# Performance work log

Hardware: AMD Instinct MI355X
Metric: run time of the kernel (lower is better)

Reference implementation:

```python
import jax, jax.numpy as jnp
import numpy as np

N_NODES = 100000
N_EDGES = 1600000
IN_DIM, HID_DIM, OUT_DIM = 32, 64, 8


def sage_conv(x, src, dst, W_l, b_l, W_r, n_nodes):
    # PyG SAGEConv (aggr='mean', root_weight=True):
    # out_i = W_l @ mean_{j in N(i)} x_j + b_l + W_r @ x_i
    msg_sum = jax.ops.segment_sum(x[src], dst, num_segments=n_nodes)  # [N, F]
    deg = jax.ops.segment_sum(jnp.ones((src.shape[0],), x.dtype), dst,
                              num_segments=n_nodes)  # [N]
    agg = msg_sum / jnp.maximum(deg, 1.0)[:, None]
    return agg @ W_l.T + b_l + x @ W_r.T


def setup_inputs() -> dict:
    key = jax.random.key(0)
    ks = jax.random.split(key, 8)
    x = jax.random.normal(ks[0], (N_NODES, IN_DIM), dtype=jnp.float32)
    edge_index = jax.random.randint(ks[1], (2, N_EDGES), 0, N_NODES, dtype=jnp.int64)
    s1 = 1.0 / np.sqrt(IN_DIM)
    s2 = 1.0 / np.sqrt(HID_DIM)
    return {
        "x": x,
        "edge_index": edge_index,
        "W1_l": jax.random.uniform(ks[2], (HID_DIM, IN_DIM), jnp.float32, -s1, s1),
        "b1": jnp.zeros((HID_DIM,), jnp.float32),
        "W1_r": jax.random.uniform(ks[3], (HID_DIM, IN_DIM), jnp.float32, -s1, s1),
        "W2_l": jax.random.uniform(ks[4], (OUT_DIM, HID_DIM), jnp.float32, -s2, s2),
        "b2": jnp.zeros((OUT_DIM,), jnp.float32),
        "W2_r": jax.random.uniform(ks[5], (OUT_DIM, HID_DIM), jnp.float32, -s2, s2),
    }


def reference(x, edge_index, W1_l, b1, W1_r, W2_l, b2, W2_r):
    src, dst = edge_index[0], edge_index[1]
    h = sage_conv(x, src, dst, W1_l, b1, W1_r, N_NODES)
    h = jax.nn.relu(h)
    out = sage_conv(h, src, dst, W2_l, b2, W2_r, N_NODES)
    return out
```

## Files before the change

kernel.cpp:

```cpp
#include <hip/hip_runtime.h>

#define N_NODES 100000
#define N_EDGES 1600000
#define IN_DIM 32
#define HID_DIM 64
#define OUT_DIM 8
#define CAP 64
#define CHUNK 4096
#define NCHUNK ((N_EDGES + CHUNK - 1) / CHUNK)
#define SLICE_W (N_NODES / 8)
#define QCAP 262144
#define BBLK 2048

typedef unsigned short u16;
typedef unsigned int u32;
typedef unsigned long long ull;

__device__ __forceinline__ float bf2f(u16 v) {
    return __uint_as_float(((u32)v) << 16);
}

__device__ __forceinline__ u16 f2bf(float f) {
    u32 u = __float_as_uint(f);
    u32 lsb = (u >> 16) & 1u;
    u += 0x7fffu + lsb;
    return (u16)(u >> 16);
}

__device__ __forceinline__ float ldf(const void* p, size_t i, int bf) {
    return bf ? bf2f(((const u16*)p)[i]) : ((const float*)p)[i];
}

__global__ __launch_bounds__(256) void k_part(
    const int* __restrict__ ei, const u32* __restrict__ xw,
    const void* __restrict__ W1l, const void* __restrict__ b1,
    const void* __restrict__ W1r,
    const void* __restrict__ W2l, const void* __restrict__ b2,
    const void* __restrict__ W2r,
    int* __restrict__ qcnt, u32* __restrict__ qbuf,
    int* __restrict__ cnt,
    float* __restrict__ tW1l, float* __restrict__ tW1r,
    float* __restrict__ tW2l, float* __restrict__ tW2r,
    float* __restrict__ tb1, float* __restrict__ tb2)
{
    __shared__ int shv, bfv;
    __shared__ int hist[4][8], wbase[4][8], lcur[4][8], gbase[8];
    int t = threadIdx.x, w = t >> 6;
    if (t < 64) {
        int v = ei[2 * t + 1];
        ull m1 = __ballot(v == 0);
        u32 wd = xw[t];
        u32 b = (wd >> 8) & 0x7fu;
        ull m2 = __ballot(b >= 0x38u && b <= 0x41u);
        if (t == 0) {
            shv = (m1 == ~0ULL) ? 1 : 0;
            bfv = (__popcll(m2) >= 56) ? 1 : 0;
        }
    }
    if (t < 32) { hist[t >> 3][t & 7] = 0; lcur[t >> 3][t & 7] = 0; }
    __syncthreads();
    int sh = shv, bf = bfv;

    for (int i = blockIdx.x * 256 + t; i < N_NODES; i += NCHUNK * 256) cnt[i] = 0;

    if (blockIdx.x < 16) {
        for (int i = blockIdx.x * 256 + t; i < HID_DIM * IN_DIM; i += 16 * 256) {
            int o = i / IN_DIM, k = i % IN_DIM;
            tW1l[k * HID_DIM + o] = ldf(W1l, i, bf);
            tW1r[k * HID_DIM + o] = ldf(W1r, i, bf);
        }
        for (int i = blockIdx.x * 256 + t; i < OUT_DIM * HID_DIM; i += 16 * 256) {
            int o = i / HID_DIM, k = i % HID_DIM;
            tW2l[k * OUT_DIM + o] = ldf(W2l, i, bf);
            tW2r[k * OUT_DIM + o] = ldf(W2r, i, bf);
        }
        if (blockIdx.x == 0) {
            if (t < HID_DIM) tb1[t] = ldf(b1, t, bf);
            if (t < OUT_DIM) tb2[t] = ldf(b2, t, bf);
        }
    }

    int e0 = blockIdx.x * CHUNK;
    int myd[16], mys[16];
    #pragma unroll
    for (int i = 0; i < 16; i++) {
        int e = e0 + i * 256 + t;
        if (e < N_EDGES) {
            size_t off = (size_t)e << sh;
            mys[i] = ei[off];
            int d = ei[((size_t)N_EDGES << sh) + off];
            myd[i] = d;
            atomicAdd(&hist[w][d / SLICE_W], 1);
        } else myd[i] = -1;
    }
    __syncthreads();
    if (t < 8) {
        int tot = hist[0][t] + hist[1][t] + hist[2][t] + hist[3][t];
        gbase[t] = atomicAdd(&qcnt[t], tot);
    }
    __syncthreads();
    if (t < 32) {
        int w2 = t >> 3, s = t & 7;
        int p = gbase[s];
        for (int w3 = 0; w3 < w2; w3++) p += hist[w3][s];
        wbase[w2][s] = p;
    }
    __syncthreads();
    #pragma unroll
    for (int i = 0; i < 16; i++) {
        int d = myd[i];
        if (d >= 0) {
            int s = d / SLICE_W;
            int p = wbase[w][s] + atomicAdd(&lcur[w][s], 1);
            qbuf[(size_t)s * QCAP + p] = ((u32)mys[i] << 14) | (u32)(d - s * SLICE_W);
        }
    }
}

__global__ __launch_bounds__(256) void k_build2(
    const int* __restrict__ qcnt, const u32* __restrict__ qbuf,
    int* __restrict__ cnt, int* __restrict__ slot)
{
    int slice = blockIdx.x & 7, bi = blockIdx.x >> 3;
    int m = qcnt[slice];
    int lo = slice * SLICE_W;
    const u32* q = qbuf + (size_t)slice * QCAP;
    for (int i = bi * 256 + threadIdx.x; i < m; i += (BBLK / 8) * 256) {
        u32 u = q[i];
        int d = lo + (int)(u & 0x3FFFu);
        int s = (int)(u >> 14);
        int pos = atomicAdd(&cnt[d], 1);
        if (pos < CAP) slot[(size_t)d * CAP + pos] = s;
    }
}

__global__ __launch_bounds__(256, 8) void k_sage1(
    const void* __restrict__ x, const int* __restrict__ cnt,
    const int* __restrict__ slot,
    const float* __restrict__ tW1l, const float* __restrict__ tW1r,
    const float* __restrict__ tW2l, const float* __restrict__ tW2r,
    const float* __restrict__ tb1, const float* __restrict__ tb2,
    const int* __restrict__ flags_unused,
    u16* __restrict__ gbuf, float* __restrict__ rbuf,
    const u32* __restrict__ xw)
{
    __shared__ float aggbuf[8][IN_DIM];
    __shared__ float xbuf[8][IN_DIM];
    __shared__ float hbuf[8][HID_DIM + 1];
    __shared__ int bfv;

    int t = threadIdx.x;
    if (t < 64) {
        u32 wd = xw[t];
        u32 b = (wd >> 8) & 0x7fu;
        ull m2 = __ballot(b >= 0x38u && b <= 0x41u);
        if (t == 0) bfv = (__popcll(m2) >= 56) ? 1 : 0;
    }
    __syncthreads();
    int bf = bfv;
    int wid = t >> 6, lane = t & 63;
    int half = lane >> 5;
    int g2 = (lane >> 3) & 3;
    int l = lane & 7;
    int ns = wid * 2 + half;
    int n = blockIdx.x * 8 + ns;
    int deg = cnt[n];
    int cl = (deg < CAP) ? deg : CAP;
    const int* srow = slot + (size_t)n * CAP;

    float a0 = 0, a1 = 0, a2 = 0, a3 = 0;
    float c0 = 0, c1 = 0, c2 = 0, c3 = 0;
    float d0 = 0, d1 = 0, d2 = 0, d3 = 0;
    float e0 = 0, e1 = 0, e2 = 0, e3 = 0;
    int j = g2;
    for (; j + 12 < cl; j += 16) {
        int sA = srow[j];
        int sB = srow[j + 4];
        int sC = srow[j + 8];
        int sD = srow[j + 12];
        if (bf) {
            ushort4 vA = reinterpret_cast<const ushort4*>((const u16*)x + (size_t)sA * IN_DIM)[l];
            ushort4 vB = reinterpret_cast<const ushort4*>((const u16*)x + (size_t)sB * IN_DIM)[l];
            ushort4 vC = reinterpret_cast<const ushort4*>((const u16*)x + (size_t)sC * IN_DIM)[l];
            ushort4 vD = reinterpret_cast<const ushort4*>((const u16*)x + (size_t)sD * IN_DIM)[l];
            a0 += bf2f(vA.x); a1 += bf2f(vA.y); a2 += bf2f(vA.z); a3 += bf2f(vA.w);
            c0 += bf2f(vB.x); c1 += bf2f(vB.y); c2 += bf2f(vB.z); c3 += bf2f(vB.w);
            d0 += bf2f(vC.x); d1 += bf2f(vC.y); d2 += bf2f(vC.z); d3 += bf2f(vC.w);
            e0 += bf2f(vD.x); e1 += bf2f(vD.y); e2 += bf2f(vD.z); e3 += bf2f(vD.w);
        } else {
            float4 vA = reinterpret_cast<const float4*>((const float*)x + (size_t)sA * IN_DIM)[l];
            float4 vB = reinterpret_cast<const float4*>((const float*)x + (size_t)sB * IN_DIM)[l];
            float4 vC = reinterpret_cast<const float4*>((const float*)x + (size_t)sC * IN_DIM)[l];
            float4 vD = reinterpret_cast<const float4*>((const float*)x + (size_t)sD * IN_DIM)[l];
            a0 += vA.x; a1 += vA.y; a2 += vA.z; a3 += vA.w;
            c0 += vB.x; c1 += vB.y; c2 += vB.z; c3 += vB.w;
            d0 += vC.x; d1 += vC.y; d2 += vC.z; d3 += vC.w;
            e0 += vD.x; e1 += vD.y; e2 += vD.z; e3 += vD.w;
        }
    }
    for (; j + 4 < cl; j += 8) {
        int sA = srow[j];
        int sB = srow[j + 4];
        if (bf) {
            ushort4 vA = reinterpret_cast<const ushort4*>((const u16*)x + (size_t)sA * IN_DIM)[l];
            ushort4 vB = reinterpret_cast<const ushort4*>((const u16*)x + (size_t)sB * IN_DIM)[l];
            a0 += bf2f(vA.x); a1 += bf2f(vA.y); a2 += bf2f(vA.z); a3 += bf2f(vA.w);
            c0 += bf2f(vB.x); c1 += bf2f(vB.y); c2 += bf2f(vB.z); c3 += bf2f(vB.w);
        } else {
            float4 vA = reinterpret_cast<const float4*>((const float*)x + (size_t)sA * IN_DIM)[l];
            float4 vB = reinterpret_cast<const float4*>((const float*)x + (size_t)sB * IN_DIM)[l];
            a0 += vA.x; a1 += vA.y; a2 += vA.z; a3 += vA.w;
            c0 += vB.x; c1 += vB.y; c2 += vB.z; c3 += vB.w;
        }
    }
    if (j < cl) {
        int s = srow[j];
        if (bf) {
            ushort4 v = reinterpret_cast<const ushort4*>((const u16*)x + (size_t)s * IN_DIM)[l];
            a0 += bf2f(v.x); a1 += bf2f(v.y); a2 += bf2f(v.z); a3 += bf2f(v.w);
        } else {
            float4 v = reinterpret_cast<const float4*>((const float*)x + (size_t)s * IN_DIM)[l];
            a0 += v.x; a1 += v.y; a2 += v.z; a3 += v.w;
        }
    }
    a0 += c0 + d0 + e0;
    a1 += c1 + d1 + e1;
    a2 += c2 + d2 + e2;
    a3 += c3 + d3 + e3;
    a0 += __shfl_xor(a0, 8, 64);  a0 += __shfl_xor(a0, 16, 64);
    a1 += __shfl_xor(a1, 8, 64);  a1 += __shfl_xor(a1, 16, 64);
    a2 += __shfl_xor(a2, 8, 64);  a2 += __shfl_xor(a2, 16, 64);
    a3 += __shfl_xor(a3, 8, 64);  a3 += __shfl_xor(a3, 16, 64);
    if (g2 == 0) {
        aggbuf[ns][4 * l + 0] = a0; aggbuf[ns][4 * l + 1] = a1;
        aggbuf[ns][4 * l + 2] = a2; aggbuf[ns][4 * l + 3] = a3;
    } else if (g2 == 1) {
        float f0, f1, f2, f3;
        if (bf) {
            ushort4 v = reinterpret_cast<const ushort4*>((const u16*)x + (size_t)n * IN_DIM)[l];
            f0 = bf2f(v.x); f1 = bf2f(v.y); f2 = bf2f(v.z); f3 = bf2f(v.w);
        } else {
            float4 v = reinterpret_cast<const float4*>((const float*)x + (size_t)n * IN_DIM)[l];
            f0 = v.x; f1 = v.y; f2 = v.z; f3 = v.w;
        }
        xbuf[ns][4 * l + 0] = f0; xbuf[ns][4 * l + 1] = f1;
        xbuf[ns][4 * l + 2] = f2; xbuf[ns][4 * l + 3] = f3;
    }
    __syncthreads();

    float rd0 = 1.0f / fmaxf((float)__shfl(deg, 0, 64), 1.0f);
    float rd1 = 1.0f / fmaxf((float)__shfl(deg, 32, 64), 1.0f);
    int s0 = wid * 2, s1 = wid * 2 + 1;
    int o = lane;
    float bb = tb1[o];
    float acc0 = bb, acc1 = bb;
    #pragma unroll 8
    for (int k = 0; k < IN_DIM; k++) {
        float wl = tW1l[k * HID_DIM + o];
        float wr = tW1r[k * HID_DIM + o];
        acc0 += (aggbuf[s0][k] * rd0) * wl + xbuf[s0][k] * wr;
        acc1 += (aggbuf[s1][k] * rd1) * wl + xbuf[s1][k] * wr;
    }
    hbuf[s0][o] = fmaxf(acc0, 0.0f);
    hbuf[s1][o] = fmaxf(acc1, 0.0f);
    __syncthreads();

    float ga = 0.0f, ra = 0.0f;
    #pragma unroll 4
    for (int m = 0; m < 16; m++) {
        int k = g2 * 16 + m;
        float hv = hbuf[ns][k];
        ga += hv * tW2l[k * OUT_DIM + l];
        ra += hv * tW2r[k * OUT_DIM + l];
    }
    ga += __shfl_xor(ga, 8, 64);  ga += __shfl_xor(ga, 16, 64);
    ra += __shfl_xor(ra, 8, 64);  ra += __shfl_xor(ra, 16, 64);
    if (g2 == 0) {
        gbuf[(size_t)n * OUT_DIM + l] = f2bf(ga);
        rbuf[(size_t)n * OUT_DIM + l] = ra + tb2[l];
    }
}

__global__ __launch_bounds__(256) void k_sage3(
    const u16* __restrict__ gbuf, const float* __restrict__ rbuf,
    const int* __restrict__ cnt, const int* __restrict__ slot,
    const u32* __restrict__ xw, void* __restrict__ out)
{
    __shared__ int bfv;
    int t = threadIdx.x;
    if (t < 64) {
        u32 w = xw[t];
        u32 b = (w >> 8) & 0x7fu;
        ull m2 = __ballot(b >= 0x38u && b <= 0x41u);
        if (t == 0) bfv = (__popcll(m2) >= 56) ? 1 : 0;
    }
    __syncthreads();
    int grp = t >> 3, l = t & 7;
    int n = blockIdx.x * 32 + grp;
    int deg = cnt[n];
    int cl = (deg < CAP) ? deg : CAP;
    const int* srow = slot + (size_t)n * CAP;
    float a0 = 0.0f, a1 = 0.0f, a2 = 0.0f, a3 = 0.0f;
    int j = 0;
    for (; j + 3 < cl; j += 4) {
        int v0 = srow[j];
        int v1 = srow[j + 1];
        int v2 = srow[j + 2];
        int v3 = srow[j + 3];
        a0 += bf2f(gbuf[(size_t)v0 * OUT_DIM + l]);
        a1 += bf2f(gbuf[(size_t)v1 * OUT_DIM + l]);
        a2 += bf2f(gbuf[(size_t)v2 * OUT_DIM + l]);
        a3 += bf2f(gbuf[(size_t)v3 * OUT_DIM + l]);
    }
    for (; j < cl; j++) a0 += bf2f(gbuf[(size_t)srow[j] * OUT_DIM + l]);
    float res = (a0 + a1 + a2 + a3) / fmaxf((float)deg, 1.0f)
              + rbuf[(size_t)n * OUT_DIM + l];
    size_t oi = (size_t)n * OUT_DIM + l;
    if (bfv) ((u16*)out)[oi] = f2bf(res);
    else     ((float*)out)[oi] = res;
}

extern "C" void kernel_launch(void* const* d_in, const int* in_sizes, int n_in,
                              void* d_out, int out_size, void* d_ws, size_t ws_size,
                              hipStream_t stream) {
    const void* x   = d_in[0];
    const int*  ei  = (const int*)d_in[1];
    const void* W1l = d_in[2];
    const void* b1  = d_in[3];
    const void* W1r = d_in[4];
    const void* W2l = d_in[5];
    const void* b2  = d_in[6];
    const void* W2r = d_in[7];

    int* qcnt    = (int*)d_ws;
    int* cnt     = qcnt + 8;
    float* tW1l  = (float*)(cnt + N_NODES);
    float* tW1r  = tW1l + IN_DIM * HID_DIM;
    float* tW2l  = tW1r + IN_DIM * HID_DIM;
    float* tW2r  = tW2l + HID_DIM * OUT_DIM;
    float* tb1   = tW2r + HID_DIM * OUT_DIM;
    float* tb2   = tb1 + HID_DIM;
    int* slot    = (int*)(tb2 + OUT_DIM);
    u32* qbuf    = (u32*)(slot + (size_t)N_NODES * CAP);
    u16* gbuf    = (u16*)(qbuf + (size_t)8 * QCAP);
    float* rbuf  = (float*)(gbuf + (size_t)N_NODES * OUT_DIM);

    hipMemsetAsync(d_ws, 0, 8 * sizeof(int), stream);

    k_part<<<NCHUNK, 256, 0, stream>>>(ei, (const u32*)x,
                                       W1l, b1, W1r, W2l, b2, W2r,
                                       qcnt, qbuf, cnt,
                                       tW1l, tW1r, tW2l, tW2r, tb1, tb2);
    k_build2<<<BBLK, 256, 0, stream>>>(qcnt, qbuf, cnt, slot);
    k_sage1<<<N_NODES / 8, 256, 0, stream>>>(x, cnt, slot, tW1l, tW1r,
                                             tW2l, tW2r, tb1, tb2, nullptr,
                                             gbuf, rbuf, (const u32*)x);
    k_sage3<<<N_NODES / 32, 256, 0, stream>>>(gbuf, rbuf, cnt, slot,
                                              (const u32*)x, d_out);
}
```

Measured before the change: 253.5 us.

## Fuse all stages into one cooperative persistent kernel with grid syncs

Replaces the four-kernel pipeline (partition, slot build, layer-1 SAGE, layer-2 aggregation) with a single cooperative kernel of 1024 persistent blocks separated by grid.sync barriers. Edge partitioning now writes into per-block, per-slice segments sized by a fixed cap instead of using global queue counters, and counter zeroing moves into the kernel. The aim is to remove kernel launch gaps and the memset. The costs are that each stage is limited to the cooperative grid's occupancy and every grid barrier is a full stall. Edges beyond the per-segment cap of 384 would be silently dropped, and the old kernels remain as a fallback if the cooperative launch fails.

Result: slower. 860.3 us (+239.4%).

```diff
diff --git a/kernel.cpp b/kernel.cpp
--- a/kernel.cpp
+++ b/kernel.cpp
@@ -1,4 +1,7 @@
 #include <hip/hip_runtime.h>
+#include <hip/hip_cooperative_groups.h>
+
+namespace cg = cooperative_groups;
 
 #define N_NODES 100000
 #define N_EDGES 1600000
@@ -6,9 +9,11 @@
 #define HID_DIM 64
 #define OUT_DIM 8
 #define CAP 64
+#define NBLK 1024
+#define SLICE_W (N_NODES / 8)
+#define SEGCAP 384
 #define CHUNK 4096
 #define NCHUNK ((N_EDGES + CHUNK - 1) / CHUNK)
-#define SLICE_W (N_NODES / 8)
 #define QCAP 262144
 #define BBLK 2048
 
@@ -31,7 +36,263 @@
     return bf ? bf2f(((const u16*)p)[i]) : ((const float*)p)[i];
 }
 
-__global__ __launch_bounds__(256) void k_part(
+__global__ __launch_bounds__(256, 4) void k_all(
+    const int* __restrict__ ei, const u32* __restrict__ xw,
+    const void* __restrict__ x,
+    const void* __restrict__ W1l, const void* __restrict__ b1,
+    const void* __restrict__ W1r,
+    const void* __restrict__ W2l, const void* __restrict__ b2,
+    const void* __restrict__ W2r,
+    int* __restrict__ cnt, int* __restrict__ qcntPB, u32* __restrict__ qbuf,
+    int* __restrict__ slot,
+    float* __restrict__ tW1l, float* __restrict__ tW1r,
+    float* __restrict__ tW2l, float* __restrict__ tW2r,
+    float* __restrict__ tb1, float* __restrict__ tb2,
+    u16* __restrict__ gbuf, float* __restrict__ rbuf,
+    void* __restrict__ out)
+{
+    __shared__ int shv, bfv;
+    __shared__ int lcnt[8];
+    __shared__ float aggbuf[8][IN_DIM];
+    __shared__ float xbuf[8][IN_DIM];
+    __shared__ float hbuf[8][HID_DIM + 1];
+
+    cg::grid_group grid = cg::this_grid();
+    int t = threadIdx.x;
+    int bid = blockIdx.x;
+
+    if (t < 64) {
+        int v = ei[2 * t + 1];
+        ull m1 = __ballot(v == 0);
+        u32 wd = xw[t];
+        u32 b = (wd >> 8) & 0x7fu;
+        ull m2 = __ballot(b >= 0x38u && b <= 0x41u);
+        if (t == 0) {
+            shv = (m1 == ~0ULL) ? 1 : 0;
+            bfv = (__popcll(m2) >= 56) ? 1 : 0;
+        }
+    }
+    if (t < 8) lcnt[t] = 0;
+    __syncthreads();
+    int sh = shv, bf = bfv;
+
+    for (int i = bid * 256 + t; i < N_NODES; i += NBLK * 256) cnt[i] = 0;
+
+    if (bid < 16) {
+        for (int i = bid * 256 + t; i < HID_DIM * IN_DIM; i += 16 * 256) {
+            int o = i / IN_DIM, k = i % IN_DIM;
+            tW1l[k * HID_DIM + o] = ldf(W1l, i, bf);
+            tW1r[k * HID_DIM + o] = ldf(W1r, i, bf);
+        }
+        for (int i = bid * 256 + t; i < OUT_DIM * HID_DIM; i += 16 * 256) {
+            int o = i / HID_DIM, k = i % HID_DIM;
+            tW2l[k * OUT_DIM + o] = ldf(W2l, i, bf);
+            tW2r[k * OUT_DIM + o] = ldf(W2r, i, bf);
+        }
+        if (bid == 0) {
+            if (t < HID_DIM) tb1[t] = ldf(b1, t, bf);
+            if (t < OUT_DIM) tb2[t] = ldf(b2, t, bf);
+        }
+    }
+
+    {
+        int e_begin = (int)((long long)bid * N_EDGES / NBLK);
+        int e_end   = (int)((long long)(bid + 1) * N_EDGES / NBLK);
+        for (int e = e_begin + t; e < e_end; e += 256) {
+            size_t off = (size_t)e << sh;
+            int s = ei[off];
+            int d = ei[((size_t)N_EDGES << sh) + off];
+            int sl = d / SLICE_W;
+            int pos = atomicAdd(&lcnt[sl], 1);
+            if (pos < SEGCAP)
+                qbuf[((size_t)sl * NBLK + bid) * SEGCAP + pos] =
+                    ((u32)s << 14) | (u32)(d - sl * SLICE_W);
+        }
+        __syncthreads();
+        if (t < 8) {
+            int c = lcnt[t];
+            qcntPB[bid * 8 + t] = (c < SEGCAP) ? c : SEGCAP;
+        }
+    }
+    __threadfence();
+    grid.sync();
+
+    {
+        int slice = bid & 7;
+        int lo = slice * SLICE_W;
+        for (int sb = bid >> 3; sb < NBLK; sb += (NBLK / 8)) {
+            int m = qcntPB[sb * 8 + slice];
+            const u32* q = qbuf + ((size_t)slice * NBLK + sb) * SEGCAP;
+            for (int i = t; i < m; i += 256) {
+                u32 u = q[i];
+                int d = lo + (int)(u & 0x3FFFu);
+                int s = (int)(u >> 14);
+                int pos = atomicAdd(&cnt[d], 1);
+                if (pos < CAP) slot[(size_t)d * CAP + pos] = s;
+            }
+        }
+    }
+    __threadfence();
+    grid.sync();
+
+    {
+        int wid = t >> 6, lane = t & 63;
+        int half = lane >> 5;
+        int g2 = (lane >> 3) & 3;
+        int l = lane & 7;
+        int ns = wid * 2 + half;
+        for (int g = bid; g < N_NODES / 8; g += NBLK) {
+            int n = g * 8 + ns;
+            int deg = cnt[n];
+            int cl = (deg < CAP) ? deg : CAP;
+            const int* srow = slot + (size_t)n * CAP;
+
+            float a0 = 0, a1 = 0, a2 = 0, a3 = 0;
+            float c0 = 0, c1 = 0, c2 = 0, c3 = 0;
+            float d0 = 0, d1 = 0, d2 = 0, d3 = 0;
+            float e0 = 0, e1 = 0, e2 = 0, e3 = 0;
+            int j = g2;
+            for (; j + 12 < cl; j += 16) {
+                int sA = srow[j];
+                int sB = srow[j + 4];
+                int sC = srow[j + 8];
+                int sD = srow[j + 12];
+                if (bf) {
+                    ushort4 vA = reinterpret_cast<const ushort4*>((const u16*)x + (size_t)sA * IN_DIM)[l];
+                    ushort4 vB = reinterpret_cast<const ushort4*>((const u16*)x + (size_t)sB * IN_DIM)[l];
+                    ushort4 vC = reinterpret_cast<const ushort4*>((const u16*)x + (size_t)sC * IN_DIM)[l];
+                    ushort4 vD = reinterpret_cast<const ushort4*>((const u16*)x + (size_t)sD * IN_DIM)[l];
+                    a0 += bf2f(vA.x); a1 += bf2f(vA.y); a2 += bf2f(vA.z); a3 += bf2f(vA.w);
+                    c0 += bf2f(vB.x); c1 += bf2f(vB.y); c2 += bf2f(vB.z); c3 += bf2f(vB.w);
+                    d0 += bf2f(vC.x); d1 += bf2f(vC.y); d2 += bf2f(vC.z); d3 += bf2f(vC.w);
+                    e0 += bf2f(vD.x); e1 += bf2f(vD.y); e2 += bf2f(vD.z); e3 += bf2f(vD.w);
+                } else {
+                    float4 vA = reinterpret_cast<const float4*>((const float*)x + (size_t)sA * IN_DIM)[l];
+                    float4 vB = reinterpret_cast<const float4*>((const float*)x + (size_t)sB * IN_DIM)[l];
+                    float4 vC = reinterpret_cast<const float4*>((const float*)x + (size_t)sC * IN_DIM)[l];
+                    float4 vD = reinterpret_cast<const float4*>((const float*)x + (size_t)sD * IN_DIM)[l];
+                    a0 += vA.x; a1 += vA.y; a2 += vA.z; a3 += vA.w;
+                    c0 += vB.x; c1 += vB.y; c2 += vB.z; c3 += vB.w;
+                    d0 += vC.x; d1 += vC.y; d2 += vC.z; d3 += vC.w;
+                    e0 += vD.x; e1 += vD.y; e2 += vD.z; e3 += vD.w;
+                }
+            }
+            for (; j + 4 < cl; j += 8) {
+                int sA = srow[j];
+                int sB = srow[j + 4];
+                if (bf) {
+                    ushort4 vA = reinterpret_cast<const ushort4*>((const u16*)x + (size_t)sA * IN_DIM)[l];
+                    ushort4 vB = reinterpret_cast<const ushort4*>((const u16*)x + (size_t)sB * IN_DIM)[l];
+                    a0 += bf2f(vA.x); a1 += bf2f(vA.y); a2 += bf2f(vA.z); a3 += bf2f(vA.w);
+                    c0 += bf2f(vB.x); c1 += bf2f(vB.y); c2 += bf2f(vB.z); c3 += bf2f(vB.w);
+                } else {
+                    float4 vA = reinterpret_cast<const float4*>((const float*)x + (size_t)sA * IN_DIM)[l];
+                    float4 vB = reinterpret_cast<const float4*>((const float*)x + (size_t)sB * IN_DIM)[l];
+                    a0 += vA.x; a1 += vA.y; a2 += vA.z; a3 += vA.w;
+                    c0 += vB.x; c1 += vB.y; c2 += vB.z; c3 += vB.w;
+                }
+            }
+            if (j < cl) {
+                int s = srow[j];
+                if (bf) {
+                    ushort4 v = reinterpret_cast<const ushort4*>((const u16*)x + (size_t)s * IN_DIM)[l];
+                    a0 += bf2f(v.x); a1 += bf2f(v.y); a2 += bf2f(v.z); a3 += bf2f(v.w);
+                } else {
+                    float4 v = reinterpret_cast<const float4*>((const float*)x + (size_t)s * IN_DIM)[l];
+                    a0 += v.x; a1 += v.y; a2 += v.z; a3 += v.w;
+                }
+            }
+            a0 += c0 + d0 + e0;
+            a1 += c1 + d1 + e1;
+            a2 += c2 + d2 + e2;
+            a3 += c3 + d3 + e3;
+            a0 += __shfl_xor(a0, 8, 64);  a0 += __shfl_xor(a0, 16, 64);
+            a1 += __shfl_xor(a1, 8, 64);  a1 += __shfl_xor(a1, 16, 64);
+            a2 += __shfl_xor(a2, 8, 64);  a2 += __shfl_xor(a2, 16, 64);
+            a3 += __shfl_xor(a3, 8, 64);  a3 += __shfl_xor(a3, 16, 64);
+            if (g2 == 0) {
+                aggbuf[ns][4 * l + 0] = a0; aggbuf[ns][4 * l + 1] = a1;
+                aggbuf[ns][4 * l + 2] = a2; aggbuf[ns][4 * l + 3] = a3;
+            } else if (g2 == 1) {
+                float f0, f1, f2, f3;
+                if (bf) {
+                    ushort4 v = reinterpret_cast<const ushort4*>((const u16*)x + (size_t)n * IN_DIM)[l];
+                    f0 = bf2f(v.x); f1 = bf2f(v.y); f2 = bf2f(v.z); f3 = bf2f(v.w);
+                } else {
+                    float4 v = reinterpret_cast<const float4*>((const float*)x + (size_t)n * IN_DIM)[l];
+                    f0 = v.x; f1 = v.y; f2 = v.z; f3 = v.w;
+                }
+                xbuf[ns][4 * l + 0] = f0; xbuf[ns][4 * l + 1] = f1;
+                xbuf[ns][4 * l + 2] = f2; xbuf[ns][4 * l + 3] = f3;
+            }
+            __syncthreads();
+
+            float rd0 = 1.0f / fmaxf((float)__shfl(deg, 0, 64), 1.0f);
+            float rd1 = 1.0f / fmaxf((float)__shfl(deg, 32, 64), 1.0f);
+            int s0 = wid * 2, s1 = wid * 2 + 1;
+            int o = lane;
+            float bb = tb1[o];
+            float acc0 = bb, acc1 = bb;
+            #pragma unroll 8
+            for (int k = 0; k < IN_DIM; k++) {
+                float wl = tW1l[k * HID_DIM + o];
+                float wr = tW1r[k * HID_DIM + o];
+                acc0 += (aggbuf[s0][k] * rd0) * wl + xbuf[s0][k] * wr;
+                acc1 += (aggbuf[s1][k] * rd1) * wl + xbuf[s1][k] * wr;
+            }
+            hbuf[s0][o] = fmaxf(acc0, 0.0f);
+            hbuf[s1][o] = fmaxf(acc1, 0.0f);
+            __syncthreads();
+
+            float ga = 0.0f, ra = 0.0f;
+            #pragma unroll 4
+            for (int m = 0; m < 16; m++) {
+                int k = g2 * 16 + m;
+                float hv = hbuf[ns][k];
+                ga += hv * tW2l[k * OUT_DIM + l];
+                ra += hv * tW2r[k * OUT_DIM + l];
+            }
+            ga += __shfl_xor(ga, 8, 64);  ga += __shfl_xor(ga, 16, 64);
+            ra += __shfl_xor(ra, 8, 64);  ra += __shfl_xor(ra, 16, 64);
+            if (g2 == 0) {
+                gbuf[(size_t)n * OUT_DIM + l] = f2bf(ga);
+                rbuf[(size_t)n * OUT_DIM + l] = ra + tb2[l];
+            }
+        }
+    }
+    __threadfence();
+    grid.sync();
+
+    {
+        int grp = t >> 3, l = t & 7;
+        for (int gg = bid; gg < N_NODES / 32; gg += NBLK) {
+            int n = gg * 32 + grp;
+            int deg = cnt[n];
+            int cl = (deg < CAP) ? deg : CAP;
+            const int* srow = slot + (size_t)n * CAP;
+            float a0 = 0.0f, a1 = 0.0f, a2 = 0.0f, a3 = 0.0f;
+            int j = 0;
+            for (; j + 3 < cl; j += 4) {
+                int v0 = srow[j];
+                int v1 = srow[j + 1];
+                int v2 = srow[j + 2];
+                int v3 = srow[j + 3];
+                a0 += bf2f(gbuf[(size_t)v0 * OUT_DIM + l]);
+                a1 += bf2f(gbuf[(size_t)v1 * OUT_DIM + l]);
+                a2 += bf2f(gbuf[(size_t)v2 * OUT_DIM + l]);
+                a3 += bf2f(gbuf[(size_t)v3 * OUT_DIM + l]);
+            }
+            for (; j < cl; j++) a0 += bf2f(gbuf[(size_t)srow[j] * OUT_DIM + l]);
+            float res = (a0 + a1 + a2 + a3) / fmaxf((float)deg, 1.0f)
+                      + rbuf[(size_t)n * OUT_DIM + l];
+            size_t oi = (size_t)n * OUT_DIM + l;
+            if (bf) ((u16*)out)[oi] = f2bf(res);
+            else    ((float*)out)[oi] = res;
+        }
+    }
+}
+
+__global__ __launch_bounds__(256) void k_part_fb(
     const int* __restrict__ ei, const u32* __restrict__ xw,
     const void* __restrict__ W1l, const void* __restrict__ b1,
     const void* __restrict__ W1r,
@@ -117,7 +378,7 @@
     }
 }
 
-__global__ __launch_bounds__(256) void k_build2(
+__global__ __launch_bounds__(256) void k_build2_fb(
     const int* __restrict__ qcnt, const u32* __restrict__ qbuf,
     int* __restrict__ cnt, int* __restrict__ slot)
 {
@@ -134,13 +395,12 @@
     }
 }
 
-__global__ __launch_bounds__(256, 8) void k_sage1(
+__global__ __launch_bounds__(256, 8) void k_sage1_fb(
     const void* __restrict__ x, const int* __restrict__ cnt,
     const int* __restrict__ slot,
     const float* __restrict__ tW1l, const float* __restrict__ tW1r,
     const float* __restrict__ tW2l, const float* __restrict__ tW2r,
     const float* __restrict__ tb1, const float* __restrict__ tb2,
-    const int* __restrict__ flags_unused,
     u16* __restrict__ gbuf, float* __restrict__ rbuf,
     const u32* __restrict__ xw)
 {
@@ -281,7 +541,7 @@
     }
 }
 
-__global__ __launch_bounds__(256) void k_sage3(
+__global__ __launch_bounds__(256) void k_sage3_fb(
     const u16* __restrict__ gbuf, const float* __restrict__ rbuf,
     const int* __restrict__ cnt, const int* __restrict__ slot,
     const u32* __restrict__ xw, void* __restrict__ out)
@@ -332,9 +592,9 @@
     const void* b2  = d_in[6];
     const void* W2r = d_in[7];
 
-    int* qcnt    = (int*)d_ws;
-    int* cnt     = qcnt + 8;
-    float* tW1l  = (float*)(cnt + N_NODES);
+    int* cnt     = (int*)d_ws;
+    int* qcntPB  = cnt + N_NODES;
+    float* tW1l  = (float*)(qcntPB + NBLK * 8);
     float* tW1r  = tW1l + IN_DIM * HID_DIM;
     float* tW2l  = tW1r + IN_DIM * HID_DIM;
     float* tW2r  = tW2l + HID_DIM * OUT_DIM;
@@ -342,19 +602,31 @@
     float* tb2   = tb1 + HID_DIM;
     int* slot    = (int*)(tb2 + OUT_DIM);
     u32* qbuf    = (u32*)(slot + (size_t)N_NODES * CAP);
-    u16* gbuf    = (u16*)(qbuf + (size_t)8 * QCAP);
+    u16* gbuf    = (u16*)(qbuf + (size_t)8 * NBLK * SEGCAP);
     float* rbuf  = (float*)(gbuf + (size_t)N_NODES * OUT_DIM);
 
-    hipMemsetAsync(d_ws, 0, 8 * sizeof(int), stream);
-
-    k_part<<<NCHUNK, 256, 0, stream>>>(ei, (const u32*)x,
-                                       W1l, b1, W1r, W2l, b2, W2r,
-                                       qcnt, qbuf, cnt,
-                                       tW1l, tW1r, tW2l, tW2r, tb1, tb2);
-    k_build2<<<BBLK, 256, 0, stream>>>(qcnt, qbuf, cnt, slot);
-    k_sage1<<<N_NODES / 8, 256, 0, stream>>>(x, cnt, slot, tW1l, tW1r,
-                                             tW2l, tW2r, tb1, tb2, nullptr,
-                                             gbuf, rbuf, (const u32*)x);
-    k_sage3<<<N_NODES / 32, 256, 0, stream>>>(gbuf, rbuf, cnt, slot,
-                                              (const u32*)x, d_out);
-}
+    const u32* xw = (const u32*)x;
+    void* args[] = {
+        (void*)&ei, (void*)&xw, (void*)&x,
+        (void*)&W1l, (void*)&b1, (void*)&W1r,
+        (void*)&W2l, (void*)&b2, (void*)&W2r,
+        (void*)&cnt, (void*)&qcntPB, (void*)&qbuf, (void*)&slot,
+        (void*)&tW1l, (void*)&tW1r, (void*)&tW2l, (void*)&tW2r,
+        (void*)&tb1, (void*)&tb2,
+        (void*)&gbuf, (void*)&rbuf, (void*)&d_out,
+    };
+    hipError_t err = hipLaunchCooperativeKernel((const void*)k_all, dim3(NBLK),
+                                                dim3(256), args, 0, stream);
+    if (err != hipSuccess) {
+        hipMemsetAsync(qcntPB, 0, 8 * sizeof(int), stream);
+        k_part_fb<<<NCHUNK, 256, 0, stream>>>(ei, xw, W1l, b1, W1r, W2l, b2, W2r,
+                                              qcntPB, qbuf, cnt,
+                                              tW1l, tW1r, tW2l, tW2r, tb1, tb2);
+        k_build2_fb<<<BBLK, 256, 0, stream>>>(qcntPB, qbuf, cnt, slot);
+        k_sage1_fb<<<N_NODES / 8, 256, 0, stream>>>(x, cnt, slot, tW1l, tW1r,
+                                                    tW2l, tW2r, tb1, tb2,
+                                                    gbuf, rbuf, xw);
+        k_sage3_fb<<<N_NODES / 32, 256, 0, stream>>>(gbuf, rbuf, cnt, slot,
+                                                     xw, d_out);
+    }
+}
```
